# Kernel optimization log

Hardware: AMD Instinct MI355X
Metric: run time of the kernel (lower is better)

Reference implementation:

```python
import jax, jax.numpy as jnp
import numpy as np

N_NODES = 20000
N_EDGES = 320000
HIDDEN = 64
HEADS = 8
HEAD_DIM = HIDDEN // HEADS
K_HOPS = 2
CST = 1e-05


def setup_inputs() -> dict:
    key = jax.random.key(0)
    ks = jax.random.split(key, 12)
    s = 1.0 / np.sqrt(HIDDEN)
    inp = {
        "x": jax.random.normal(ks[0], (N_NODES, HIDDEN), dtype=jnp.float32),
        "edge_index": jax.random.randint(ks[1], (2, N_EDGES), 0, N_NODES, dtype=jnp.int64),
        "edge_feature": jnp.zeros((1,), dtype=jnp.float32),  # unused by the module
        "Wq": jax.random.uniform(ks[2], (HIDDEN, HIDDEN), jnp.float32, -s, s),
        "bq": jax.random.uniform(ks[3], (HIDDEN,), jnp.float32, -s, s),
        "Wk": jax.random.uniform(ks[4], (HIDDEN, HIDDEN), jnp.float32, -s, s),
        "bk": jax.random.uniform(ks[5], (HIDDEN,), jnp.float32, -s, s),
        "Wv": jax.random.uniform(ks[6], (HIDDEN, HIDDEN), jnp.float32, -s, s),
        "bv": jax.random.uniform(ks[7], (HIDDEN,), jnp.float32, -s, s),
        "Wo": jax.random.uniform(ks[8], (HIDDEN, HIDDEN), jnp.float32, -s, s),
        "bo": jax.random.uniform(ks[9], (HIDDEN,), jnp.float32, -s, s),
        "hopwise": jnp.ones((K_HOPS + 1,), dtype=jnp.float32),
        "headwise": jnp.zeros((HEADS, K_HOPS), dtype=jnp.float32),
    }
    return inp


def reference(x, edge_index, edge_feature, Wq, bq, Wk, bk, Wv, bv, Wo, bo, hopwise, headwise):
    N = x.shape[0]
    row, col = edge_index[0], edge_index[1]

    # symmetric normalization: deg is in-degree of col
    deg = jax.ops.segment_sum(jnp.ones_like(col, dtype=x.dtype), col, num_segments=N)
    deg_inv = jnp.where(deg > 0, deg ** -0.5, 0.0)
    norm = deg_inv[row] * deg_inv[col]  # [E]

    Q = 1.0 + jax.nn.elu(x @ Wq + bq)
    K = 1.0 + jax.nn.elu(x @ Wk + bk)
    V = (x @ Wv + bv)
    Q = Q.reshape(N, HEADS, HEAD_DIM)
    K = K.reshape(N, HEADS, HEAD_DIM)
    V = V.reshape(N, HEADS, HEAD_DIM)

    M = jnp.einsum('nhi,nhj->nhij', K, V)  # [N,H,d,d]
    hidden = V * hopwise[0]
    layerwise = jax.nn.softmax(headwise, axis=0)  # softmax over heads (dim=-2)

    for hop in range(K_HOPS):
        # scatter-add propagation: out[i] = sum_{e: col[e]=i} norm[e] * state[row[e]]
        M = jax.ops.segment_sum(norm[:, None, None, None] * M[row], col, num_segments=N)
        K = jax.ops.segment_sum(norm[:, None, None] * K[row], col, num_segments=N)
        H = jnp.einsum('nhi,nhij->nhj', Q, M)
        C = jnp.einsum('nhi,nhi->nh', Q, K)[..., None] + CST
        H = H / C
        gamma = hopwise[hop + 1] * layerwise[:, hop][:, None]  # [H,1]
        hidden = hidden + gamma * H

    hidden = hidden.reshape(N, HEADS * HEAD_DIM)
    # dropout is identity in eval mode
    return hidden @ Wo + bo
```

## Files before the change

kernel.cpp:

```cpp
#include <hip/hip_runtime.h>
#include <hip/hip_bf16.h>

typedef __hip_bfloat16 bf16;
typedef __fp16 half2_t __attribute__((ext_vector_type(2)));
typedef float floatx2 __attribute__((ext_vector_type(2)));

#define N_NODES 20000
#define N_EDGES 320000
#define CSTF 1e-5f

#if defined(__has_builtin)
#if __has_builtin(__builtin_amdgcn_cvt_pk_fp8_f32) && __has_builtin(__builtin_amdgcn_cvt_pk_f32_fp8)
#define M1FP8 1
#endif
#if __has_builtin(__builtin_amdgcn_fdot2)
#define HAVE_FDOT2 1
#endif
#endif

#ifdef M1FP8
#define M1_STRIDE 128
#define M1_LANE   2
typedef uint2 m1vec;
#else
#define M1_STRIDE 256
#define M1_LANE   4
typedef uint4 m1vec;
#endif

__device__ __forceinline__ half2_t u2h(unsigned int u) {
    union { unsigned int u; half2_t h; } c; c.u = u; return c.h;
}
__device__ __forceinline__ unsigned int pkh(float a, float b) {
    union { __fp16 h[2]; unsigned int u; } c;
    c.h[0] = (__fp16)a; c.h[1] = (__fp16)b;
    return c.u;
}
__device__ __forceinline__ float fdot2(half2_t a, half2_t b, float c) {
#ifdef HAVE_FDOT2
    return __builtin_amdgcn_fdot2(a, b, c, false);
#else
    return fmaf((float)a.x, (float)b.x, fmaf((float)a.y, (float)b.y, c));
#endif
}
__device__ __forceinline__ int rdl(int v, int lane) { return __builtin_amdgcn_readlane(v, lane); }
__device__ __forceinline__ float ldf(const void* p, int i, bool bf) {
    return bf ? __bfloat162float(((const bf16*)p)[i]) : ((const float*)p)[i];
}
__device__ __forceinline__ bool wave_is_i64(const void* ei, int e) {
    unsigned int hi = ((const unsigned int*)ei)[2 * e + 1];
    return !__any(hi != 0);
}

struct Args {
    const void *x, *ei, *Wq, *bq, *Wk, *bk, *Wv, *bv, *Wo, *bo, *hopwise, *headwise;
    void* out;
    float* Q;
    _Float16 *K0h, *Vh, *K1h;
    unsigned int* M1h;
    int* bsrc;
    float* gbuf;
    int *deg, *cnt;
};

__global__ __launch_bounds__(256) void k_p1(Args a) {
    const int t = threadIdx.x;
    const int e = blockIdx.x * 256 + t;
    bool i64 = wave_is_i64(a.ei, e);
    int r, c;
    if (i64) {
        r = (int)((const long long*)a.ei)[e];
        c = (int)((const long long*)a.ei)[N_EDGES + e];
    } else {
        r = ((const int*)a.ei)[e];
        c = ((const int*)a.ei)[N_EDGES + e];
    }
    int slot = atomicAdd(&a.deg[c], 1);
    if (slot < 64) a.bsrc[c * 64 + slot] = r;
    if (blockIdx.x < 64) {
        int bad = 0;
        for (int i = blockIdx.x * 256 + t; i < 40000; i += 64 * 256) {
            unsigned int w = ((const unsigned int*)a.x)[i];
            if (((w >> 7)  & 0xFFu) == 0xFFu) bad++;
            if (((w >> 23) & 0xFFu) == 0xFFu) bad++;
        }
        if (bad) atomicAdd(&a.cnt[0], bad);
    }
}

__global__ __launch_bounds__(256) void k_p2(Args a) {
    __shared__ __fp16 sWh[3 * 4096];
    __shared__ float sx[8][64];
    const int t = threadIdx.x;
    const bool bf = (a.cnt[0] < 16);
    const int n0 = blockIdx.x * 8;
    for (int i = t; i < 4096; i += 256) {
        int k = i >> 6, col = i & 63;
        int di_ = (k >> 1) * 128 + col * 2 + (k & 1);
        sWh[di_]        = (__fp16)ldf(a.Wq, i, bf);
        sWh[4096 + di_] = (__fp16)ldf(a.Wk, i, bf);
        sWh[8192 + di_] = (__fp16)ldf(a.Wv, i, bf);
    }
    for (int i = t; i < 512; i += 256) {
        int row = i >> 6, col = i & 63;
        sx[row][col] = ldf(a.x, (n0 + row) * 64 + col, bf);
    }
    if (blockIdx.x == 0 && t < 8) {
        float e0 = 0.0f, e1 = 0.0f;
        for (int hh = 0; hh < 8; hh++) {
            e0 += __expf(ldf(a.headwise, hh * 2 + 0, bf));
            e1 += __expf(ldf(a.headwise, hh * 2 + 1, bf));
        }
        float hw1 = ldf(a.hopwise, 1, bf), hw2 = ldf(a.hopwise, 2, bf);
        a.gbuf[t]     = hw1 * __expf(ldf(a.headwise, t * 2 + 0, bf)) / e0;
        a.gbuf[8 + t] = hw2 * __expf(ldf(a.headwise, t * 2 + 1, bf)) / e1;
        if (t == 0) a.gbuf[16] = ldf(a.hopwise, 0, bf);
    }
    __syncthreads();
    const unsigned int* sWq = (const unsigned int*)sWh;
    const unsigned int* sWk = sWq + 2048;
    const unsigned int* sWv = sWq + 4096;
    const int l = t & 63, sub = t >> 6;
    const float bqv = ldf(a.bq, l, bf), bkv = ldf(a.bk, l, bf), bvv = ldf(a.bv, l, bf);
    for (int g = 0; g < 2; g++) {
        int row = g * 4 + sub;
        int n = n0 + row;
        float q = bqv, k = bkv, v = bvv;
        const float2* xp = (const float2*)sx[row];
#pragma unroll 8
        for (int kp = 0; kp < 32; kp++) {
            float2 xv = xp[kp];
            half2_t xh = u2h(pkh(xv.x, xv.y));
            q = fdot2(xh, u2h(sWq[kp * 64 + l]), q);
            k = fdot2(xh, u2h(sWk[kp * 64 + l]), k);
            v = fdot2(xh, u2h(sWv[kp * 64 + l]), v);
        }
        int dg = a.deg[n];
        float di = dg > 0 ? rsqrtf((float)dg) : 0.0f;
        a.Q[n * 64 + l] = q > 0.0f ? q + 1.0f : __expf(q);
        float kel = k > 0.0f ? k + 1.0f : __expf(k);
        a.K0h[n * 64 + l] = (_Float16)(di * kel);
        a.Vh[n * 64 + l]  = (_Float16)v;
    }
}

__global__ __launch_bounds__(128) void k_hop1(Args a) {
    const int l = threadIdx.x & 63;
    const int n = blockIdx.x * 2 + (threadIdx.x >> 6);
    const int hb = l & 56;
    float acc[8] = {0, 0, 0, 0, 0, 0, 0, 0};
    float kacc = 0.0f;
    const int dg = a.deg[n];
    const int m = min(dg, 64);
    if (m > 0) {
        const int srcv = a.bsrc[n * 64 + (l < m ? l : m - 1)];
#define H1_ACC(KU, VO, KO)                                                 \
    {                                                                      \
        half2_t p0 = u2h(KU.x), p1 = u2h(KU.y), p2 = u2h(KU.z), p3 = u2h(KU.w); \
        float vv = (float)VO;                                              \
        acc[0] = fmaf(vv, (float)p0.x, acc[0]); acc[1] = fmaf(vv, (float)p0.y, acc[1]); \
        acc[2] = fmaf(vv, (float)p1.x, acc[2]); acc[3] = fmaf(vv, (float)p1.y, acc[3]); \
        acc[4] = fmaf(vv, (float)p2.x, acc[4]); acc[5] = fmaf(vv, (float)p2.y, acc[5]); \
        acc[6] = fmaf(vv, (float)p3.x, acc[6]); acc[7] = fmaf(vv, (float)p3.y, acc[7]); \
        kacc += (float)KO;                                                 \
    }
        int e = 0;
        for (; e + 8 <= m; e += 8) {
            int s_[8];
            uint4 k_[8];
            __fp16 v_[8], o_[8];
#pragma unroll
            for (int u = 0; u < 8; u++) s_[u] = rdl(srcv, e + u);
#pragma unroll
            for (int u = 0; u < 8; u++) k_[u] = *(const uint4*)(a.K0h + s_[u] * 64 + hb);
#pragma unroll
            for (int u = 0; u < 8; u++) v_[u] = a.Vh[s_[u] * 64 + l];
#pragma unroll
            for (int u = 0; u < 8; u++) o_[u] = a.K0h[s_[u] * 64 + l];
#pragma unroll
            for (int u = 0; u < 8; u++) H1_ACC(k_[u], v_[u], o_[u])
        }
        for (; e < m; e++) {
            int sA = rdl(srcv, e);
            uint4 kA = *(const uint4*)(a.K0h + sA * 64 + hb);
            __fp16 vA = a.Vh[sA * 64 + l];
            __fp16 oA = a.K0h[sA * 64 + l];
            H1_ACC(kA, vA, oA)
        }
#undef H1_ACC
        float inv = 1.0f / (float)dg;
#pragma unroll
        for (int i = 0; i < 8; i++) acc[i] *= inv;
        kacc *= inv;
    }
#ifdef M1FP8
    unsigned int w0 = 0, w1 = 0;
    w0 = __builtin_amdgcn_cvt_pk_fp8_f32(acc[0], acc[1], w0, false);
    w0 = __builtin_amdgcn_cvt_pk_fp8_f32(acc[2], acc[3], w0, true);
    w1 = __builtin_amdgcn_cvt_pk_fp8_f32(acc[4], acc[5], w1, false);
    w1 = __builtin_amdgcn_cvt_pk_fp8_f32(acc[6], acc[7], w1, true);
    uint2 o2; o2.x = w0; o2.y = w1;
    *(uint2*)(a.M1h + (size_t)n * M1_STRIDE + l * M1_LANE) = o2;
#else
    uint4 o;
    o.x = pkh(acc[0], acc[1]); o.y = pkh(acc[2], acc[3]);
    o.z = pkh(acc[4], acc[5]); o.w = pkh(acc[6], acc[7]);
    *(uint4*)(a.M1h + (size_t)n * M1_STRIDE + l * M1_LANE) = o;
#endif
    a.K1h[n * 64 + l] = (_Float16)kacc;
}

__global__ __launch_bounds__(128) void k_hop2f(Args a) {
    __shared__ unsigned int sWo[2048];
    __shared__ float sh[2][64];
    __shared__ unsigned int shp[2][32];
    const bool bf = (a.cnt[0] < 16);
    const int t = threadIdx.x;
    const int l = t & 63;
    const int w = t >> 6;
    const int n = blockIdx.x * 2 + w;
    const int hb = l & 56, h = l >> 3;
    for (int i = t; i < 2048; i += 128) {
        int kp = i >> 6, c = i & 63;
        sWo[i] = pkh(ldf(a.Wo, 2 * kp * 64 + c, bf), ldf(a.Wo, (2 * kp + 1) * 64 + c, bf));
    }
    const float4 qa = *(const float4*)(a.Q + n * 64 + hb);
    const float4 qb = *(const float4*)(a.Q + n * 64 + hb + 4);
    const float qown = a.Q[n * 64 + l];
    float hacc = 0.0f, sk = 0.0f;
    const int dg = a.deg[n];
    const int m = min(dg, 64);
#ifdef M1FP8
#define H2_DOT(MU, DST)                                                    \
    {                                                                      \
        floatx2 a0 = __builtin_amdgcn_cvt_pk_f32_fp8(MU.x, false);         \
        floatx2 a1 = __builtin_amdgcn_cvt_pk_f32_fp8(MU.x, true);          \
        floatx2 a2 = __builtin_amdgcn_cvt_pk_f32_fp8(MU.y, false);         \
        floatx2 a3 = __builtin_amdgcn_cvt_pk_f32_fp8(MU.y, true);          \
        DST = qa.x * a0.x;                                                 \
        DST = fmaf(qa.y, a0.y, DST); DST = fmaf(qa.z, a1.x, DST);          \
        DST = fmaf(qa.w, a1.y, DST); DST = fmaf(qb.x, a2.x, DST);          \
        DST = fmaf(qb.y, a2.y, DST); DST = fmaf(qb.z, a3.x, DST);          \
        DST = fmaf(qb.w, a3.y, DST);                                       \
    }
#else
    const half2_t q01 = u2h(pkh(qa.x, qa.y));
    const half2_t q23 = u2h(pkh(qa.z, qa.w));
    const half2_t q45 = u2h(pkh(qb.x, qb.y));
    const half2_t q67 = u2h(pkh(qb.z, qb.w));
#define H2_DOT(MU, DST)                                                    \
    {                                                                      \
        DST = fdot2(q01, u2h(MU.x), 0.0f);                                 \
        DST = fdot2(q23, u2h(MU.y), DST);                                  \
        DST = fdot2(q45, u2h(MU.z), DST);                                  \
        DST = fdot2(q67, u2h(MU.w), DST);                                  \
    }
#endif
    if (m > 0) {
        const int srcv = a.bsrc[n * 64 + (l < m ? l : m - 1)];
        int e = 0;
        for (; e + 8 <= m; e += 8) {
            int s_[8];
            m1vec m_[8];
            __fp16 k_[8];
#pragma unroll
            for (int u = 0; u < 8; u++) s_[u] = rdl(srcv, e + u);
#pragma unroll
            for (int u = 0; u < 8; u++) m_[u] = *(const m1vec*)(a.M1h + (size_t)s_[u] * M1_STRIDE + l * M1_LANE);
#pragma unroll
            for (int u = 0; u < 8; u++) k_[u] = a.K1h[s_[u] * 64 + l];
#pragma unroll
            for (int u = 0; u < 8; u++) {
                float d;
                H2_DOT(m_[u], d)
                hacc += d;
                sk += (float)k_[u];
            }
        }
        for (; e < m; e++) {
            int sA = rdl(srcv, e);
            m1vec mA = *(const m1vec*)(a.M1h + (size_t)sA * M1_STRIDE + l * M1_LANE);
            __fp16 kA = a.K1h[sA * 64 + l];
            float d;
            H2_DOT(mA, d)
            hacc += d;
            sk += (float)kA;
        }
    }
    m1vec mo = *(const m1vec*)(a.M1h + (size_t)n * M1_STRIDE + l * M1_LANE);
    float h1r;
    H2_DOT(mo, h1r)
#undef H2_DOT
    const float din = dg > 0 ? rsqrtf((float)dg) : 0.0f;
    const float sq  = dg > 0 ? sqrtf((float)dg)  : 0.0f;
    float h1 = h1r * sq;
    float c1 = qown * (float)a.K1h[n * 64 + l];
    float c2 = qown * sk;
#pragma unroll
    for (int dd = 1; dd < 8; dd <<= 1) {
        c1 += __shfl_xor(c1, dd);
        c2 += __shfl_xor(c2, dd);
    }
    c1 *= sq;
    c2 *= din;
    float H2v = hacc * din;

    const float hw0 = a.gbuf[16];
    const float g1 = a.gbuf[h];
    const float g2 = a.gbuf[8 + h];
    float hidden = hw0 * (float)a.Vh[n * 64 + l] + g1 * h1 / (c1 + CSTF) + g2 * H2v / (c2 + CSTF);

    sh[w][l] = hidden;
    __syncthreads();
    if (l < 32) {
        float2 hp = *(const float2*)&sh[w][2 * l];
        shp[w][l] = pkh(hp.x, hp.y);
    }
    __syncthreads();
    float o = ldf(a.bo, l, bf);
#pragma unroll 8
    for (int kp = 0; kp < 32; kp++) {
        o = fdot2(u2h(shp[w][kp]), u2h(sWo[kp * 64 + l]), o);
    }
    if (bf) ((bf16*)a.out)[n * 64 + l] = __float2bfloat16(o);
    else    ((float*)a.out)[n * 64 + l] = o;
}

extern "C" void kernel_launch(void* const* d_in, const int* in_sizes, int n_in,
                              void* d_out, int out_size, void* d_ws, size_t ws_size,
                              hipStream_t stream) {
    char* p = (char*)d_ws;
    auto alloc = [&](size_t bytes) {
        void* r = (void*)p;
        p += (bytes + 255) & ~(size_t)255;
        return r;
    };
    Args a;
    a.x = d_in[0];  a.ei = d_in[1];
    a.Wq = d_in[3]; a.bq = d_in[4];
    a.Wk = d_in[5]; a.bk = d_in[6];
    a.Wv = d_in[7]; a.bv = d_in[8];
    a.Wo = d_in[9]; a.bo = d_in[10];
    a.hopwise = d_in[11]; a.headwise = d_in[12];
    a.out = d_out;

    a.Q    = (float*)alloc((size_t)N_NODES * 64 * 4);
    a.K0h  = (_Float16*)alloc((size_t)N_NODES * 64 * 2);
    a.Vh   = (_Float16*)alloc((size_t)N_NODES * 64 * 2);
    a.K1h  = (_Float16*)alloc((size_t)N_NODES * 64 * 2);
    a.M1h  = (unsigned int*)alloc((size_t)N_NODES * 1024);
    a.bsrc = (int*)alloc((size_t)N_NODES * 64 * 4);
    a.gbuf = (float*)alloc(32 * 4);
    int* zz = (int*)alloc(((size_t)N_NODES + 64) * 4);
    a.deg = zz;
    a.cnt = zz + N_NODES;

    (void)hipMemsetAsync(zz, 0, ((size_t)N_NODES + 64) * 4, stream);

    const int EB = (N_EDGES + 255) / 256;
    k_p1<<<EB, 256, 0, stream>>>(a);
    k_p2<<<2500, 256, 0, stream>>>(a);
    k_hop1<<<N_NODES / 2, 128, 0, stream>>>(a);
    k_hop2f<<<N_NODES / 2, 128, 0, stream>>>(a);
}
```

Measured before the change: 201.5 us.

## Sum neighbor M rows before Q dot and drop LDS Wo staging in hop2

The hop-2 kernel now accumulates the unpacked neighbor M values into per-lane vector sums and applies the Q dot product once after the loop, instead of doing a dot product per edge. This relies on linearity and removes per-edge FMAs. The output projection no longer stages Wo into shared memory with block barriers. Each lane now broadcasts hidden values by wave shuffle and reads Wo directly from global memory, which trades LDS setup and syncs for 64 global or cached loads per lane.

```diff
diff --git a/kernel.cpp b/kernel.cpp
--- a/kernel.cpp
+++ b/kernel.cpp
@@ -211,26 +211,28 @@
 }
 
 __global__ __launch_bounds__(128) void k_hop2f(Args a) {
-    __shared__ unsigned int sWo[2048];
-    __shared__ float sh[2][64];
-    __shared__ unsigned int shp[2][32];
     const bool bf = (a.cnt[0] < 16);
     const int t = threadIdx.x;
     const int l = t & 63;
-    const int w = t >> 6;
-    const int n = blockIdx.x * 2 + w;
+    const int n = blockIdx.x * 2 + (t >> 6);
     const int hb = l & 56, h = l >> 3;
-    for (int i = t; i < 2048; i += 128) {
-        int kp = i >> 6, c = i & 63;
-        sWo[i] = pkh(ldf(a.Wo, 2 * kp * 64 + c, bf), ldf(a.Wo, (2 * kp + 1) * 64 + c, bf));
-    }
     const float4 qa = *(const float4*)(a.Q + n * 64 + hb);
     const float4 qb = *(const float4*)(a.Q + n * 64 + hb + 4);
     const float qown = a.Q[n * 64 + l];
-    float hacc = 0.0f, sk = 0.0f;
     const int dg = a.deg[n];
     const int m = min(dg, 64);
+    floatx2 s01 = {0, 0}, s23 = {0, 0}, s45 = {0, 0}, s67 = {0, 0};
+    float sk = 0.0f;
+
 #ifdef M1FP8
+#define H2_ACC(MU, KO)                                                     \
+    {                                                                      \
+        s01 += __builtin_amdgcn_cvt_pk_f32_fp8(MU.x, false);               \
+        s23 += __builtin_amdgcn_cvt_pk_f32_fp8(MU.x, true);                \
+        s45 += __builtin_amdgcn_cvt_pk_f32_fp8(MU.y, false);               \
+        s67 += __builtin_amdgcn_cvt_pk_f32_fp8(MU.y, true);                \
+        sk += (float)KO;                                                   \
+    }
 #define H2_DOT(MU, DST)                                                    \
     {                                                                      \
         floatx2 a0 = __builtin_amdgcn_cvt_pk_f32_fp8(MU.x, false);         \
@@ -244,6 +246,16 @@
         DST = fmaf(qb.w, a3.y, DST);                                       \
     }
 #else
+    const half2_t one2 = u2h(pkh(1.0f, 1.0f));
+#define H2_ACC(MU, KO)                                                     \
+    {                                                                      \
+        half2_t p0 = u2h(MU.x), p1 = u2h(MU.y), p2 = u2h(MU.z), p3 = u2h(MU.w); \
+        s01.x += (float)p0.x; s01.y += (float)p0.y;                        \
+        s23.x += (float)p1.x; s23.y += (float)p1.y;                        \
+        s45.x += (float)p2.x; s45.y += (float)p2.y;                        \
+        s67.x += (float)p3.x; s67.y += (float)p3.y;                        \
+        sk += (float)KO;                                                   \
+    }
     const half2_t q01 = u2h(pkh(qa.x, qa.y));
     const half2_t q23 = u2h(pkh(qa.z, qa.w));
     const half2_t q45 = u2h(pkh(qb.x, qb.y));
@@ -256,6 +268,7 @@
         DST = fdot2(q67, u2h(MU.w), DST);                                  \
     }
 #endif
+
     if (m > 0) {
         const int srcv = a.bsrc[n * 64 + (l < m ? l : m - 1)];
         int e = 0;
@@ -270,23 +283,21 @@
 #pragma unroll
             for (int u = 0; u < 8; u++) k_[u] = a.K1h[s_[u] * 64 + l];
 #pragma unroll
-            for (int u = 0; u < 8; u++) {
-                float d;
-                H2_DOT(m_[u], d)
-                hacc += d;
-                sk += (float)k_[u];
-            }
+            for (int u = 0; u < 8; u++) H2_ACC(m_[u], k_[u])
         }
         for (; e < m; e++) {
             int sA = rdl(srcv, e);
             m1vec mA = *(const m1vec*)(a.M1h + (size_t)sA * M1_STRIDE + l * M1_LANE);
             __fp16 kA = a.K1h[sA * 64 + l];
-            float d;
-            H2_DOT(mA, d)
-            hacc += d;
-            sk += (float)kA;
-        }
-    }
+            H2_ACC(mA, kA)
+        }
+    }
+#undef H2_ACC
+    float hacc = qa.x * s01.x;
+    hacc = fmaf(qa.y, s01.y, hacc); hacc = fmaf(qa.z, s23.x, hacc);
+    hacc = fmaf(qa.w, s23.y, hacc); hacc = fmaf(qb.x, s45.x, hacc);
+    hacc = fmaf(qb.y, s45.y, hacc); hacc = fmaf(qb.z, s67.x, hacc);
+    hacc = fmaf(qb.w, s67.y, hacc);
     m1vec mo = *(const m1vec*)(a.M1h + (size_t)n * M1_STRIDE + l * M1_LANE);
     float h1r;
     H2_DOT(mo, h1r)
@@ -310,17 +321,11 @@
     const float g2 = a.gbuf[8 + h];
     float hidden = hw0 * (float)a.Vh[n * 64 + l] + g1 * h1 / (c1 + CSTF) + g2 * H2v / (c2 + CSTF);
 
-    sh[w][l] = hidden;
-    __syncthreads();
-    if (l < 32) {
-        float2 hp = *(const float2*)&sh[w][2 * l];
-        shp[w][l] = pkh(hp.x, hp.y);
-    }
-    __syncthreads();
     float o = ldf(a.bo, l, bf);
-#pragma unroll 8
-    for (int kp = 0; kp < 32; kp++) {
-        o = fdot2(u2h(shp[w][kp]), u2h(sWo[kp * 64 + l]), o);
+#pragma unroll 16
+    for (int k = 0; k < 64; k++) {
+        float hk = __shfl(hidden, k);
+        o += hk * ldf(a.Wo, k * 64 + l, bf);
     }
     if (bf) ((bf16*)a.out)[n * 64 + l] = __float2bfloat16(o);
     else    ((float*)a.out)[n * 64 + l] = o;
```

After: 194.3 us. 1.04x faster.
